# Optimization experiments

Measured on AMD Instinct MI355X. Metric: run time of the kernel, lower is better.

The kernel has to match this reference:

```python
import jax, jax.numpy as jnp
import numpy as np

DIM = 1024
HEAD_SIZE = 128
B, N = 4, 4096

def setup_inputs() -> dict:
    key = jax.random.key(0)
    kx, kq, kk, kv = jax.random.split(key, 4)
    s = (1.0 / DIM) ** 0.5  # ~ torch Linear init scale
    return {
        "x": jax.random.normal(kx, (B, N, DIM), dtype=jnp.float32),
        "Wq": jax.random.uniform(kq, (HEAD_SIZE, DIM), dtype=jnp.float32, minval=-s, maxval=s),
        "Wk": jax.random.uniform(kk, (HEAD_SIZE, DIM), dtype=jnp.float32, minval=-s, maxval=s),
        "Wv": jax.random.uniform(kv, (HEAD_SIZE, DIM), dtype=jnp.float32, minval=-s, maxval=s),
    }

def reference(x, Wq, Wk, Wv):
    # x: [B, N, dim]; W*: [head_size, dim] (torch Linear convention y = x @ W.T)
    q = jnp.einsum('bnd,hd->bnh', x, Wq)
    k = jnp.einsum('bnd,hd->bnh', x, Wk)
    v = jnp.einsum('bnd,hd->bnh', x, Wv)
    scale = DIM ** (-0.5)  # NOTE: original scales by dim**-0.5, not head_size
    scores = jnp.einsum('bnh,bmh->bnm', q, k) * scale  # [B, N, N]
    weights = jax.nn.softmax(scores, axis=-1)
    context = jnp.einsum('bnm,bmh->bnh', weights, v)  # [B, N, head_size]
    return context
```

## Files before the change

kernel.cpp:

```cpp
#include <hip/hip_runtime.h>

using bf16x8   = __attribute__((ext_vector_type(8))) __bf16;
using f32x4    = __attribute__((ext_vector_type(4))) float;
using f32x16   = __attribute__((ext_vector_type(16))) float;
using floatv4  = __attribute__((ext_vector_type(4))) float;
using ushortv4 = __attribute__((ext_vector_type(4))) unsigned short;
using ushortv8 = __attribute__((ext_vector_type(8))) unsigned short;
using uintv4   = __attribute__((ext_vector_type(4))) unsigned int;

#define N_SEQ 4096
#define N_B   4
#define DIMK  1024
#define HS    128
#define ROWS  (N_B * N_SEQ)
#define KVB   32

__device__ __forceinline__ unsigned short f2bf(float f) {
    unsigned u = __builtin_bit_cast(unsigned, f);
    u += 0x7FFFu + ((u >> 16) & 1u);
    return (unsigned short)(u >> 16);
}

__device__ __forceinline__ unsigned cvtpk(float lo, float hi) {
    unsigned r;
    asm("v_cvt_pk_bf16_f32 %0, %1, %2" : "=v"(r) : "v"(lo), "v"(hi));
    return r;
}

__device__ __forceinline__ void gload16(const unsigned short* g, unsigned short* l) {
    __builtin_amdgcn_global_load_lds(
        (const __attribute__((address_space(1))) unsigned int*)g,
        (__attribute__((address_space(3))) unsigned int*)l, 16, 0, 0);
}

__global__ __launch_bounds__(256) void cast_kernel(
    const float* __restrict__ X,
    const float* __restrict__ Wq,
    const float* __restrict__ Wk,
    const float* __restrict__ Wv,
    unsigned short* __restrict__ Xb,
    unsigned short* __restrict__ Wb)
{
    const int blk = blockIdx.x;
    const float* src;
    unsigned short* dst;
    size_t off;
    if (blk < 8192) {
        src = X; dst = Xb; off = (size_t)blk * 2048;
    } else {
        int wblk = blk - 8192;
        int z = wblk >> 6;
        src = (z == 0) ? Wq : (z == 1) ? Wk : Wv;
        dst = Wb + (size_t)z * (HS * DIMK);
        off = (size_t)(wblk & 63) * 2048;
    }
    size_t i = off + (size_t)threadIdx.x * 8;
    floatv4 a = *reinterpret_cast<const floatv4*>(src + i);
    floatv4 b = *reinterpret_cast<const floatv4*>(src + i + 4);
    ushortv8 o = { f2bf(a.x), f2bf(a.y), f2bf(a.z), f2bf(a.w),
                   f2bf(b.x), f2bf(b.y), f2bf(b.z), f2bf(b.w) };
    *reinterpret_cast<ushortv8*>(dst + i) = o;
}

__global__ __launch_bounds__(256, 3) void proj_kernel(
    const unsigned short* __restrict__ Xb,
    const unsigned short* __restrict__ Wb,
    unsigned short* __restrict__ Qb,
    unsigned short* __restrict__ Kb,
    unsigned short* __restrict__ Vt)
{
    const int z = blockIdx.y;
    const unsigned short* __restrict__ Wz = Wb + (size_t)z * (HS * DIMK);
    const int row0 = blockIdx.x * 64;
    __shared__ unsigned short smem[2 * 64 * 64 + 2 * 128 * 64];
    unsigned short* Xs0 = smem;
    unsigned short* Ws0 = smem + 2 * 64 * 64;
    const int tid = threadIdx.x;
    const int wv = tid >> 6, lane = tid & 63;
    const int lr = lane & 15, lg = lane >> 4;

    f32x4 acc[4][2] = {};

    auto stage = [&](int buf, int k0) {
        #pragma unroll
        for (int i = 0; i < 2; ++i) {
            int g = wv * 2 + i;
            int r = g * 8 + (lane >> 3);
            int sp = (lane & 7) ^ (r & 7);
            gload16(Xb + (size_t)(row0 + r) * DIMK + k0 + sp * 8,
                    Xs0 + buf * (64 * 64) + g * 8 * 64);
        }
        #pragma unroll
        for (int i = 0; i < 4; ++i) {
            int g = wv * 4 + i;
            int r = g * 8 + (lane >> 3);
            int sp = (lane & 7) ^ (r & 7);
            gload16(Wz + (size_t)r * DIMK + k0 + sp * 8,
                    Ws0 + buf * (128 * 64) + g * 8 * 64);
        }
    };

    stage(0, 0);
    __syncthreads();
    for (int ks = 0; ks < DIMK / 64; ++ks) {
        const int cur = ks & 1;
        if (ks < DIMK / 64 - 1) stage(cur ^ 1, (ks + 1) * 64);
        const unsigned short* Xc = Xs0 + cur * (64 * 64);
        const unsigned short* Wc = Ws0 + cur * (128 * 64);
        bf16x8 af[4][2], bfr[2][2];
        #pragma unroll
        for (int mi = 0; mi < 4; ++mi)
            #pragma unroll
            for (int kk = 0; kk < 2; ++kk)
                af[mi][kk] = *reinterpret_cast<const bf16x8*>(
                    &Xc[(mi * 16 + lr) * 64 + (((kk * 4 + lg) ^ (lr & 7)) * 8)]);
        #pragma unroll
        for (int ni = 0; ni < 2; ++ni)
            #pragma unroll
            for (int kk = 0; kk < 2; ++kk)
                bfr[ni][kk] = *reinterpret_cast<const bf16x8*>(
                    &Wc[(wv * 32 + ni * 16 + lr) * 64 + (((kk * 4 + lg) ^ (lr & 7)) * 8)]);
        #pragma unroll
        for (int kk = 0; kk < 2; ++kk)
            #pragma unroll
            for (int mi = 0; mi < 4; ++mi)
                #pragma unroll
                for (int ni = 0; ni < 2; ++ni)
                    acc[mi][ni] = __builtin_amdgcn_mfma_f32_16x16x32_bf16(
                        af[mi][kk], bfr[ni][kk], acc[mi][ni], 0, 0, 0);
        __syncthreads();
    }

    if (z < 2) {
        unsigned short* O = (z == 0) ? Qb : Kb;
        #pragma unroll
        for (int mi = 0; mi < 4; ++mi) {
            int rowb = row0 + mi * 16 + lg * 4;
            #pragma unroll
            for (int ni = 0; ni < 2; ++ni) {
                int col = wv * 32 + ni * 16 + lr;
                #pragma unroll
                for (int r = 0; r < 4; ++r)
                    O[(size_t)(rowb + r) * HS + col] = f2bf(acc[mi][ni][r]);
            }
        }
    } else {
        unsigned short* Cs = smem;
        #pragma unroll
        for (int mi = 0; mi < 4; ++mi)
            #pragma unroll
            for (int ni = 0; ni < 2; ++ni)
                #pragma unroll
                for (int r = 0; r < 4; ++r)
                    Cs[(mi * 16 + lg * 4 + r) * 132 + wv * 32 + ni * 16 + lr] = f2bf(acc[mi][ni][r]);
        __syncthreads();
        const int b  = row0 >> 12;
        const int n0 = row0 & (N_SEQ - 1);
        #pragma unroll
        for (int i = 0; i < 4; ++i) {
            int idx = tid + i * 256;
            int d = idx >> 3, c8 = idx & 7;
            ushortv8 v;
            #pragma unroll
            for (int j = 0; j < 8; ++j)
                v[j] = Cs[(c8 * 8 + j) * 132 + d];
            *reinterpret_cast<ushortv8*>(Vt + (size_t)b * HS * N_SEQ + (size_t)d * N_SEQ + n0 + c8 * 8) = v;
        }
    }
}

__global__ __launch_bounds__(256, 3) void attn_kernel(
    const unsigned short* __restrict__ Qb,
    const unsigned short* __restrict__ Kb,
    const unsigned short* __restrict__ Vt,
    unsigned short* __restrict__ part,
    float* __restrict__ plsum,
    int S)
{
    const int qblk  = blockIdx.x;
    const int split = blockIdx.y;
    const int tid = threadIdx.x;
    const int wv = tid >> 6, lane = tid & 63;
    const int l31 = lane & 31, h = lane >> 5;
    const int b    = qblk >> 5;
    const int row0 = (qblk & 31) * 128 + wv * 32;

    __shared__ unsigned short Ks[2][KVB * 128];
    __shared__ unsigned short Vs[2][128 * KVB];

    bf16x8 qf[8];
    {
        const unsigned short* qp = Qb + ((size_t)b * N_SEQ + row0 + l31) * HS + h * 8;
        #pragma unroll
        for (int kk = 0; kk < 8; ++kk)
            qf[kk] = *reinterpret_cast<const bf16x8*>(qp + kk * 16);
    }

    const int kvlen = N_SEQ / S;
    const int nt = kvlen / KVB;
    const int kv_begin = split * kvlen;
    const unsigned short* Kbb = Kb + (size_t)b * N_SEQ * HS;
    const unsigned short* Vbb = Vt + (size_t)b * HS * N_SEQ;

    auto stage = [&](int buf, int kv0) {
        #pragma unroll
        for (int i = 0; i < 2; ++i) {
            int g = wv * 2 + i;
            int r = g * 4 + (lane >> 4);
            int sp = (lane & 15) ^ (r & 7);
            gload16(Kbb + (size_t)(kv0 + r) * HS + sp * 8, &Ks[buf][g * 4 * 128]);
        }
        #pragma unroll
        for (int i = 0; i < 2; ++i) {
            int g = wv * 2 + i;
            int r = g * 16 + (lane >> 2);
            int sp = (lane & 3) ^ ((r >> 1) & 3);
            gload16(Vbb + (size_t)r * N_SEQ + kv0 + sp * 8, &Vs[buf][g * 16 * KVB]);
        }
    };

    f32x16 ctx[4] = {};
    f32x16 lacc = {};
    const ushortv8 ones_u = {0x3F80,0x3F80,0x3F80,0x3F80,0x3F80,0x3F80,0x3F80,0x3F80};
    const bf16x8 onesf = __builtin_bit_cast(bf16x8, ones_u);
    const float CEXP = 0.045084220027780106f;

    stage(0, kv_begin);
    __syncthreads();
    for (int t = 0; t < nt; ++t) {
        const int cur = t & 1;
        if (t + 1 < nt) stage(cur ^ 1, kv_begin + (t + 1) * KVB);

        f32x16 st = {};
        #pragma unroll
        for (int kk = 0; kk < 8; ++kk) {
            bf16x8 kf = *reinterpret_cast<const bf16x8*>(
                &Ks[cur][l31 * 128 + (((kk * 2 + h) ^ (l31 & 7)) * 8)]);
            st = __builtin_amdgcn_mfma_f32_32x32x16_bf16(kf, qf[kk], st, 0, 0, 0);
        }

        float p[16];
        #pragma unroll
        for (int r = 0; r < 16; ++r)
            p[r] = exp2f(st[r] * CEXP);

        bf16x8 pf[2];
        #pragma unroll
        for (int half = 0; half < 2; ++half) {
            unsigned a = cvtpk(p[half*8 + 0], p[half*8 + 1]);
            unsigned bq = cvtpk(p[half*8 + 2], p[half*8 + 3]);
            unsigned c = cvtpk(p[half*8 + 4], p[half*8 + 5]);
            unsigned d = cvtpk(p[half*8 + 6], p[half*8 + 7]);
            asm("v_permlane32_swap_b32 %0, %1" : "+v"(a), "+v"(c));
            asm("v_permlane32_swap_b32 %0, %1" : "+v"(bq), "+v"(d));
            uintv4 w = { a, bq, c, d };
            pf[half] = __builtin_bit_cast(bf16x8, w);
        }

        lacc = __builtin_amdgcn_mfma_f32_32x32x16_bf16(pf[0], onesf, lacc, 0, 0, 0);
        lacc = __builtin_amdgcn_mfma_f32_32x32x16_bf16(pf[1], onesf, lacc, 0, 0, 0);

        #pragma unroll
        for (int dt = 0; dt < 4; ++dt) {
            int d = dt * 32 + l31;
            bf16x8 vf0 = *reinterpret_cast<const bf16x8*>(
                &Vs[cur][d * KVB + (((0 + h) ^ ((d >> 1) & 3)) * 8)]);
            ctx[dt] = __builtin_amdgcn_mfma_f32_32x32x16_bf16(pf[0], vf0, ctx[dt], 0, 0, 0);
            bf16x8 vf1 = *reinterpret_cast<const bf16x8*>(
                &Vs[cur][d * KVB + (((2 + h) ^ ((d >> 1) & 3)) * 8)]);
            ctx[dt] = __builtin_amdgcn_mfma_f32_32x32x16_bf16(pf[1], vf1, ctx[dt], 0, 0, 0);
        }
        __syncthreads();
    }

    const int qt = qblk * 4 + wv;
    unsigned short* pp = part + ((size_t)qt * S + split) * (32 * 128);
    #pragma unroll
    for (int rp = 0; rp < 4; ++rp)
        #pragma unroll
        for (int rq = 0; rq < 4; ++rq) {
            const int r = rp * 4 + rq;
            const int q = rq + 8 * rp + 4 * h;
            #pragma unroll
            for (int dt = 0; dt < 4; ++dt)
                pp[q * 128 + dt * 32 + l31] = (unsigned short)(cvtpk(ctx[dt][r], ctx[dt][r]) & 0xFFFFu);
        }
    if (l31 == 0) {
        float* pl = plsum + ((size_t)qt * S + split) * 32;
        #pragma unroll
        for (int rp = 0; rp < 4; ++rp)
            #pragma unroll
            for (int rq = 0; rq < 4; ++rq)
                pl[rq + 8 * rp + 4 * h] = lacc[rp * 4 + rq];
    }
}

__global__ __launch_bounds__(256) void reduce_kernel(
    const unsigned short* __restrict__ part,
    const float* __restrict__ plsum,
    float* __restrict__ out, int S)
{
    const int id = blockIdx.x * 256 + threadIdx.x;
    const int d4 = (id & 31) * 4;
    const int grow = id >> 5;
    const int qt = grow >> 5, q = grow & 31;
    f32x4 c = {0.f, 0.f, 0.f, 0.f};
    float l = 0.f;
    for (int s = 0; s < S; ++s) {
        ushortv4 pv = *reinterpret_cast<const ushortv4*>(
            &part[(((size_t)qt * S + s) * 32 + q) * 128 + d4]);
        #pragma unroll
        for (int j = 0; j < 4; ++j)
            c[j] += __builtin_bit_cast(float, (unsigned)pv[j] << 16);
        l += plsum[((size_t)qt * S + s) * 32 + q];
    }
    float inv = 1.0f / l;
    f32x4 o = { c[0]*inv, c[1]*inv, c[2]*inv, c[3]*inv };
    *reinterpret_cast<f32x4*>(&out[(size_t)grow * 128 + d4]) = o;
}

extern "C" void kernel_launch(void* const* d_in, const int* in_sizes, int n_in,
                              void* d_out, int out_size, void* d_ws, size_t ws_size,
                              hipStream_t stream) {
    const float* x  = (const float*)d_in[0];
    const float* wq = (const float*)d_in[1];
    const float* wk = (const float*)d_in[2];
    const float* wv = (const float*)d_in[3];

    unsigned short* Xb = (unsigned short*)d_ws;
    unsigned short* Wb = Xb + (size_t)ROWS * DIMK;
    unsigned short* Qb = Wb + (size_t)3 * HS * DIMK;
    unsigned short* Kb = Qb + (size_t)ROWS * HS;
    unsigned short* Vt = Kb + (size_t)ROWS * HS;
    float* plsum = (float*)(Vt + (size_t)N_B * HS * N_SEQ);
    unsigned short* part = (unsigned short*)d_ws;

    const size_t base = ((size_t)ROWS * DIMK + 3 * HS * DIMK + 3 * (size_t)ROWS * HS) * 2;
    int S;
    if      (ws_size >= base + 8 * (size_t)512 * 32 * 4) S = 8;
    else if (ws_size >= base + 4 * (size_t)512 * 32 * 4) S = 4;
    else if (ws_size >= base + 2 * (size_t)512 * 32 * 4) S = 2;
    else                                                 S = 1;

    cast_kernel<<<8192 + 192, 256, 0, stream>>>(x, wq, wk, wv, Xb, Wb);
    proj_kernel<<<dim3(256, 3), 256, 0, stream>>>(Xb, Wb, Qb, Kb, Vt);
    attn_kernel<<<dim3(128, S), 256, 0, stream>>>(Qb, Kb, Vt, part, plsum, S);
    reduce_kernel<<<(ROWS * HS) / 1024, 256, 0, stream>>>(part, plsum, (float*)d_out, S);
}
```

Before: 94.06 us.

## Triple-buffer KV tiles, fold softmax scale into Q, use S=6 split

Moves the softmax scale and log2e factor into the Q projection output so the attention loop calls a raw hardware exp2 with no per-element multiply. Replaces the double-buffered K/V staging with a three-slot ring, using explicit vmcnt waits and one barrier per iteration instead of two syncthreads. Raises MFMA priority around the matrix sections and changes the KV split count from 8 to 6, with uneven tile distribution across splits. This trades extra LDS, which may lower occupancy, for deeper load/compute overlap and a different balance across CUs. Scaling Q before the bf16 rounding also slightly changes numerics.

```diff
diff --git a/kernel.cpp b/kernel.cpp
--- a/kernel.cpp
+++ b/kernel.cpp
@@ -14,6 +14,7 @@
 #define HS    128
 #define ROWS  (N_B * N_SEQ)
 #define KVB   32
+#define TT    (N_SEQ / KVB)
 
 __device__ __forceinline__ unsigned short f2bf(float f) {
     unsigned u = __builtin_bit_cast(unsigned, f);
@@ -133,6 +134,7 @@
 
     if (z < 2) {
         unsigned short* O = (z == 0) ? Qb : Kb;
+        const float qs = (z == 0) ? 0.045084220027780106f : 1.0f;
         #pragma unroll
         for (int mi = 0; mi < 4; ++mi) {
             int rowb = row0 + mi * 16 + lg * 4;
@@ -141,7 +143,7 @@
                 int col = wv * 32 + ni * 16 + lr;
                 #pragma unroll
                 for (int r = 0; r < 4; ++r)
-                    O[(size_t)(rowb + r) * HS + col] = f2bf(acc[mi][ni][r]);
+                    O[(size_t)(rowb + r) * HS + col] = f2bf(acc[mi][ni][r] * qs);
             }
         }
     } else {
@@ -185,8 +187,8 @@
     const int b    = qblk >> 5;
     const int row0 = (qblk & 31) * 128 + wv * 32;
 
-    __shared__ unsigned short Ks[2][KVB * 128];
-    __shared__ unsigned short Vs[2][128 * KVB];
+    __shared__ unsigned short Ks[3][KVB * 128];
+    __shared__ unsigned short Vs[3][128 * KVB];
 
     bf16x8 qf[8];
     {
@@ -196,9 +198,10 @@
             qf[kk] = *reinterpret_cast<const bf16x8*>(qp + kk * 16);
     }
 
-    const int kvlen = N_SEQ / S;
-    const int nt = kvlen / KVB;
-    const int kv_begin = split * kvlen;
+    const int base = TT / S, rem = TT % S;
+    const int nt = base + (split < rem ? 1 : 0);
+    const int kv_begin = (split * base + (split < rem ? split : rem)) * KVB;
+
     const unsigned short* Kbb = Kb + (size_t)b * N_SEQ * HS;
     const unsigned short* Vbb = Vt + (size_t)b * HS * N_SEQ;
 
@@ -223,43 +226,51 @@
     f32x16 lacc = {};
     const ushortv8 ones_u = {0x3F80,0x3F80,0x3F80,0x3F80,0x3F80,0x3F80,0x3F80,0x3F80};
     const bf16x8 onesf = __builtin_bit_cast(bf16x8, ones_u);
-    const float CEXP = 0.045084220027780106f;
 
     stage(0, kv_begin);
-    __syncthreads();
+    stage(1, kv_begin + KVB);
+    int cur = 0, nxt = 2;
     for (int t = 0; t < nt; ++t) {
-        const int cur = t & 1;
-        if (t + 1 < nt) stage(cur ^ 1, kv_begin + (t + 1) * KVB);
+        if (t + 2 < nt) {
+            asm volatile("s_waitcnt vmcnt(4)\n\ts_barrier" ::: "memory");
+            stage(nxt, kv_begin + (t + 2) * KVB);
+        } else if (t + 1 < nt) {
+            asm volatile("s_waitcnt vmcnt(4)\n\ts_barrier" ::: "memory");
+        } else {
+            asm volatile("s_waitcnt vmcnt(0)\n\ts_barrier" ::: "memory");
+        }
 
         f32x16 st = {};
+        __builtin_amdgcn_s_setprio(1);
         #pragma unroll
         for (int kk = 0; kk < 8; ++kk) {
             bf16x8 kf = *reinterpret_cast<const bf16x8*>(
                 &Ks[cur][l31 * 128 + (((kk * 2 + h) ^ (l31 & 7)) * 8)]);
             st = __builtin_amdgcn_mfma_f32_32x32x16_bf16(kf, qf[kk], st, 0, 0, 0);
         }
+        __builtin_amdgcn_s_setprio(0);
 
         float p[16];
         #pragma unroll
         for (int r = 0; r < 16; ++r)
-            p[r] = exp2f(st[r] * CEXP);
+            p[r] = __builtin_amdgcn_exp2f(st[r]);
 
         bf16x8 pf[2];
         #pragma unroll
         for (int half = 0; half < 2; ++half) {
-            unsigned a = cvtpk(p[half*8 + 0], p[half*8 + 1]);
+            unsigned a  = cvtpk(p[half*8 + 0], p[half*8 + 1]);
             unsigned bq = cvtpk(p[half*8 + 2], p[half*8 + 3]);
-            unsigned c = cvtpk(p[half*8 + 4], p[half*8 + 5]);
-            unsigned d = cvtpk(p[half*8 + 6], p[half*8 + 7]);
+            unsigned c  = cvtpk(p[half*8 + 4], p[half*8 + 5]);
+            unsigned d  = cvtpk(p[half*8 + 6], p[half*8 + 7]);
             asm("v_permlane32_swap_b32 %0, %1" : "+v"(a), "+v"(c));
             asm("v_permlane32_swap_b32 %0, %1" : "+v"(bq), "+v"(d));
             uintv4 w = { a, bq, c, d };
             pf[half] = __builtin_bit_cast(bf16x8, w);
         }
 
+        __builtin_amdgcn_s_setprio(1);
         lacc = __builtin_amdgcn_mfma_f32_32x32x16_bf16(pf[0], onesf, lacc, 0, 0, 0);
         lacc = __builtin_amdgcn_mfma_f32_32x32x16_bf16(pf[1], onesf, lacc, 0, 0, 0);
-
         #pragma unroll
         for (int dt = 0; dt < 4; ++dt) {
             int d = dt * 32 + l31;
@@ -270,7 +281,10 @@
                 &Vs[cur][d * KVB + (((2 + h) ^ ((d >> 1) & 3)) * 8)]);
             ctx[dt] = __builtin_amdgcn_mfma_f32_32x32x16_bf16(pf[1], vf1, ctx[dt], 0, 0, 0);
         }
-        __syncthreads();
+        __builtin_amdgcn_s_setprio(0);
+
+        cur = (cur == 2) ? 0 : cur + 1;
+        nxt = (nxt == 2) ? 0 : nxt + 1;
     }
 
     const int qt = qblk * 4 + wv;
@@ -337,7 +351,7 @@
 
     const size_t base = ((size_t)ROWS * DIMK + 3 * HS * DIMK + 3 * (size_t)ROWS * HS) * 2;
     int S;
-    if      (ws_size >= base + 8 * (size_t)512 * 32 * 4) S = 8;
+    if      (ws_size >= base + 6 * (size_t)512 * 32 * 4) S = 6;
     else if (ws_size >= base + 4 * (size_t)512 * 32 * 4) S = 4;
     else if (ws_size >= base + 2 * (size_t)512 * 32 * 4) S = 2;
     else                                                 S = 1;
```

After: 83.57 us. 1.13x faster.
